# Optimization experiments

Hardware: AMD Instinct MI355X
Metric: run time of the kernel (lower is better)

## Reference

```python
import jax, jax.numpy as jnp
import numpy as np

EPS = 1e-10
COMMITMENT_COST = 0.25


def setup_inputs() -> dict:
    key = jax.random.key(0)
    k1, k2, k3, k4 = jax.random.split(key, 4)
    return {
        "x": jax.random.normal(k1, (32, 64, 64, 64), dtype=jnp.float32),  # NCHW, C=D=64
        "emb0": jax.random.normal(k2, (512, 64), dtype=jnp.float32),
        "emb1": jax.random.normal(k3, (512, 64), dtype=jnp.float32),
        "emb2": jax.random.normal(k4, (512, 64), dtype=jnp.float32),
        "idx": 1,
    }


def reference(x, emb0, emb1, emb2, idx):
    # NCHW -> NHWC, flatten to [N, D]
    inputs = jnp.transpose(x, (0, 2, 3, 1))
    in_shape = inputs.shape
    D = in_shape[-1]
    flat = inputs.reshape(-1, D)  # [N, D]

    if idx == 0:
        codes = emb0
    elif idx == 1:
        codes = jnp.concatenate([emb0, emb1], axis=0)
    else:
        codes = jnp.concatenate([emb0, emb2], axis=0)  # [K, D]

    distances = (
        jnp.sum(flat * flat, axis=1, keepdims=True)
        + jnp.sum(codes * codes, axis=1)
        - 2.0 * jnp.matmul(flat, codes.T)
    )
    enc_idx = jnp.argmin(distances, axis=1)  # [N]

    # one-hot @ codes is just a gather
    quantized = codes[enc_idx].reshape(in_shape)

    e_latent_loss = jnp.mean((jax.lax.stop_gradient(quantized) - inputs) ** 2)
    q_latent_loss = jnp.mean((quantized - jax.lax.stop_gradient(inputs)) ** 2)
    loss = q_latent_loss + COMMITMENT_COST * e_latent_loss

    # straight-through estimator
    quantized_st = inputs + jax.lax.stop_gradient(quantized - inputs)

    K = codes.shape[0]
    N = flat.shape[0]
    avg_probs = jnp.zeros((K,), dtype=flat.dtype).at[enc_idx].add(1.0) / N
    perplexity = jnp.exp(-jnp.sum(avg_probs * jnp.log(avg_probs + EPS)))

    return jnp.transpose(quantized_st, (0, 3, 1, 2)), loss, perplexity
```

## Files before the change

### kernel.cpp

```cpp
#include <hip/hip_runtime.h>
#include <math.h>

#define NROWS   131072
#define DFEAT   64
#define KHALF   512
#define HW      4096
#define CHW     262144
#define NQOUT   8388608
#define NBLK    512

typedef __attribute__((ext_vector_type(8))) short   bf16x8;
typedef __attribute__((ext_vector_type(4))) float   f32x4;

__device__ __forceinline__ unsigned short f2bf(float f) {
    unsigned int u = __float_as_uint(f);
    u += 0x7FFFu + ((u >> 16) & 1u);
    return (unsigned short)(u >> 16);
}
__device__ __forceinline__ float bf2f(unsigned short h) {
    return __uint_as_float(((unsigned int)h) << 16);
}

__global__ void vq_prep(const float* __restrict__ e0, const float* __restrict__ e1,
                        const float* __restrict__ e2, const int* __restrict__ idxp,
                        float* __restrict__ wsf, float* __restrict__ cnh,
                        unsigned short* __restrict__ fragbuf) {
    int tau = blockIdx.x * 256 + threadIdx.x;
    if (tau < 1536) wsf[tau] = 0.f;

    int idx = idxp[0];
    const float* sel = (idx == 2) ? e2 : e1;

    if (tau < 1024) {
        const float* row = (tau < KHALF) ? (e0 + (size_t)tau * DFEAT)
                                         : (sel + (size_t)(tau - KHALF) * DFEAT);
        float s = 0.f;
#pragma unroll
        for (int c = 0; c < DFEAT; ++c) s = fmaf(row[c], row[c], s);
        cnh[tau] = 0.5f * s;
    }

    int tile = tau >> 8;
    int rem  = tau & 255;
    int f    = rem >> 6;
    int L    = rem & 63;
    int code = tile * 16 + (L & 15);
    int kb   = (f & 1) * 32 + (L >> 4) * 8;
    int lo_f = f >> 1;
    const float* src = (code < KHALF) ? (e0 + (size_t)code * DFEAT)
                                      : (sel + (size_t)(code - KHALF) * DFEAT);
    unsigned short* dst = fragbuf + (size_t)tau * 8;
#pragma unroll
    for (int j = 0; j < 8; ++j) {
        float v = src[kb + j];
        unsigned short hb = f2bf(v);
        dst[j] = lo_f ? f2bf(v - bf2f(hb)) : hb;
    }
}

#define TILE_STEP(BC0, BC1, BC2, BC3, CNC, BN0, BN1, BN2, BN3, CNN, TT, TL)   \
    {                                                                          \
        const int tl_ = (TL);                                                  \
        BN0 = fb[(tl_ * 4 + 0) * 64 + L];                                      \
        BN1 = fb[(tl_ * 4 + 1) * 64 + L];                                      \
        BN2 = fb[(tl_ * 4 + 2) * 64 + L];                                      \
        BN3 = fb[(tl_ * 4 + 3) * 64 + L];                                      \
        CNN = cnh[tl_ * 16 + m];                                               \
        const int kt_ = (TT) * 16 + m;                                         \
        _Pragma("unroll")                                                      \
        for (int rt = 0; rt < 4; ++rt) {                                       \
            f32x4 acc = {0.f, 0.f, 0.f, 0.f};                                  \
            acc = __builtin_amdgcn_mfma_f32_16x16x32_bf16(ahi[rt][0], BC0, acc, 0, 0, 0); \
            acc = __builtin_amdgcn_mfma_f32_16x16x32_bf16(ahi[rt][1], BC1, acc, 0, 0, 0); \
            acc = __builtin_amdgcn_mfma_f32_16x16x32_bf16(ahi[rt][0], BC2, acc, 0, 0, 0); \
            acc = __builtin_amdgcn_mfma_f32_16x16x32_bf16(ahi[rt][1], BC3, acc, 0, 0, 0); \
            acc = __builtin_amdgcn_mfma_f32_16x16x32_bf16(alo[rt][0], BC0, acc, 0, 0, 0); \
            acc = __builtin_amdgcn_mfma_f32_16x16x32_bf16(alo[rt][1], BC1, acc, 0, 0, 0); \
            acc = __builtin_amdgcn_mfma_f32_16x16x32_bf16(alo[rt][0], BC2, acc, 0, 0, 0); \
            acc = __builtin_amdgcn_mfma_f32_16x16x32_bf16(alo[rt][1], BC3, acc, 0, 0, 0); \
            _Pragma("unroll")                                                  \
            for (int r = 0; r < 4; ++r) {                                      \
                float s = acc[r] - CNC;                                        \
                if (s > best[rt * 4 + r]) { best[rt * 4 + r] = s; bidx[rt * 4 + r] = kt_; } \
            }                                                                  \
        }                                                                      \
    }

__global__ __launch_bounds__(256, 2) void vq_main(
        const float* __restrict__ x,
        const float* __restrict__ e0, const float* __restrict__ e1,
        const float* __restrict__ e2, const int* __restrict__ idxp,
        const float* __restrict__ cnh, const unsigned short* __restrict__ fragbuf,
        float* __restrict__ out, float* __restrict__ loss_acc,
        int* __restrict__ hist) {
    __shared__ float xsq_s[256];
    __shared__ float sc_s[256];
    __shared__ int   bk_s[256];

    const int t = threadIdx.x;
    const int w = t >> 6;
    const int L = t & 63;
    const int q = L >> 4;
    const int m = L & 15;

    const int rowbase = blockIdx.x * 256;
    const int n  = rowbase >> 12;
    const int s0 = rowbase & 4095;

    const int idx = idxp[0];
    const float* sel = (idx == 2) ? e2 : e1;
    const int ntiles = (idx == 0) ? 32 : 64;

    bf16x8 ahi[4][2], alo[4][2];
    const float* xb = x + (size_t)n * CHW + (s0 + w * 64);
#pragma unroll
    for (int rt = 0; rt < 4; ++rt) {
        const float* xr = xb + rt * 16 + m;
        float xs = 0.f;
#pragma unroll
        for (int h = 0; h < 2; ++h) {
#pragma unroll
            for (int j = 0; j < 8; ++j) {
                int c = h * 32 + q * 8 + j;
                float v = xr[(size_t)c * HW];
                xs = fmaf(v, v, xs);
                unsigned short hb = f2bf(v);
                unsigned short lb = f2bf(v - bf2f(hb));
                ahi[rt][h][j] = (short)hb;
                alo[rt][h][j] = (short)lb;
            }
        }
        xs += __shfl_xor(xs, 16, 64);
        xs += __shfl_xor(xs, 32, 64);
        if (q == 0) xsq_s[w * 64 + rt * 16 + m] = xs;
    }

    const bf16x8* fb = (const bf16x8*)fragbuf;
    float best[16];
    int   bidx[16];
#pragma unroll
    for (int i = 0; i < 16; ++i) { best[i] = -3.4e38f; bidx[i] = 0; }

    bf16x8 X0 = fb[0 * 64 + L];
    bf16x8 X1 = fb[1 * 64 + L];
    bf16x8 X2 = fb[2 * 64 + L];
    bf16x8 X3 = fb[3 * 64 + L];
    float  Xc = cnh[m];
    bf16x8 Y0, Y1, Y2, Y3;
    float  Yc;

    for (int tt = 0; tt < ntiles; tt += 2) {
        TILE_STEP(X0, X1, X2, X3, Xc, Y0, Y1, Y2, Y3, Yc, tt, tt + 1);
        const int t2 = (tt + 2 < ntiles) ? tt + 2 : ntiles - 1;
        TILE_STEP(Y0, Y1, Y2, Y3, Yc, X0, X1, X2, X3, Xc, tt + 1, t2);
    }

#pragma unroll
    for (int i = 0; i < 16; ++i) {
        float b = best[i]; int k = bidx[i];
#pragma unroll
        for (int off = 1; off < 16; off <<= 1) {
            float ob = __shfl_xor(b, off, 64);
            int   ok = __shfl_xor(k, off, 64);
            if (ob > b || (ob == b && ok < k)) { b = ob; k = ok; }
        }
        if (m == 0) {
            int row = w * 64 + (i >> 2) * 16 + q * 4 + (i & 3);
            sc_s[row] = b; bk_s[row] = k;
        }
    }
    __syncthreads();

    const int k   = bk_s[t];
    float dist    = xsq_s[t] - 2.f * sc_s[t];
    float l = dist;
#pragma unroll
    for (int off = 32; off > 0; off >>= 1) l += __shfl_down(l, off, 64);
    if (L == 0) atomicAdd(loss_acc, l);
    atomicAdd(&hist[k], 1);

    const float* cp = (k < KHALF) ? (e0 + (size_t)k * DFEAT)
                                  : (sel + (size_t)(k - KHALF) * DFEAT);
    const float4* cp4 = (const float4*)cp;
    float* op = out + (size_t)n * CHW + (s0 + t);
#pragma unroll
    for (int c4 = 0; c4 < 16; ++c4) {
        float4 v = cp4[c4];
        op[(size_t)(4 * c4 + 0) * HW] = v.x;
        op[(size_t)(4 * c4 + 1) * HW] = v.y;
        op[(size_t)(4 * c4 + 2) * HW] = v.z;
        op[(size_t)(4 * c4 + 3) * HW] = v.w;
    }
}

__global__ void vq_finalize(const float* __restrict__ wsf, const int* __restrict__ hist,
                            float* __restrict__ out) {
    __shared__ double partial[16];
    const int t = threadIdx.x;
    double p = (double)hist[t] / (double)NROWS;
    double term = p * log(p + 1e-10);
#pragma unroll
    for (int off = 32; off > 0; off >>= 1) term += __shfl_down(term, off, 64);
    if ((t & 63) == 0) partial[t >> 6] = term;
    __syncthreads();
    if (t == 0) {
        double s = 0.0;
        for (int i = 0; i < 16; ++i) s += partial[i];
        out[NQOUT + 1] = (float)exp(-s);
        out[NQOUT]     = 1.25f * (wsf[0] / (float)NQOUT);
    }
}

extern "C" void kernel_launch(void* const* d_in, const int* in_sizes, int n_in,
                              void* d_out, int out_size, void* d_ws, size_t ws_size,
                              hipStream_t stream) {
    const float* x  = (const float*)d_in[0];
    const float* e0 = (const float*)d_in[1];
    const float* e1 = (const float*)d_in[2];
    const float* e2 = (const float*)d_in[3];
    const int* idxp = (const int*)d_in[4];
    float* out = (float*)d_out;

    float* wsf      = (float*)d_ws;
    float* loss_acc = wsf;
    int*   hist     = (int*)(wsf + 256);
    float* cnh      = wsf + 2048;
    unsigned short* fragbuf = (unsigned short*)(wsf + 4096);

    vq_prep<<<64, 256, 0, stream>>>(e0, e1, e2, idxp, wsf, cnh, fragbuf);
    vq_main<<<NBLK, 256, 0, stream>>>(x, e0, e1, e2, idxp, cnh, fragbuf,
                                      out, loss_acc, hist);
    vq_finalize<<<1, 1024, 0, stream>>>(wsf, hist, out);
}
```

Measured before the change: 183.5 us.

## Split codebook scan across two wave groups per block and merge argmin

```diff
diff --git a/kernel.cpp b/kernel.cpp
--- a/kernel.cpp
+++ b/kernel.cpp
@@ -86,7 +86,7 @@
         }                                                                      \
     }
 
-__global__ __launch_bounds__(256, 2) void vq_main(
+__global__ __launch_bounds__(512, 4) void vq_main(
         const float* __restrict__ x,
         const float* __restrict__ e0, const float* __restrict__ e1,
         const float* __restrict__ e2, const int* __restrict__ idxp,
@@ -94,14 +94,16 @@
         float* __restrict__ out, float* __restrict__ loss_acc,
         int* __restrict__ hist) {
     __shared__ float xsq_s[256];
-    __shared__ float sc_s[256];
-    __shared__ int   bk_s[256];
-
-    const int t = threadIdx.x;
-    const int w = t >> 6;
-    const int L = t & 63;
-    const int q = L >> 4;
-    const int m = L & 15;
+    __shared__ float sc_s[512];
+    __shared__ int   bk_s[512];
+
+    const int t  = threadIdx.x;
+    const int w  = t >> 6;
+    const int wg = w >> 2;
+    const int wv = w & 3;
+    const int L  = t & 63;
+    const int q  = L >> 4;
+    const int m  = L & 15;
 
     const int rowbase = blockIdx.x * 256;
     const int n  = rowbase >> 12;
@@ -110,9 +112,11 @@
     const int idx = idxp[0];
     const float* sel = (idx == 2) ? e2 : e1;
     const int ntiles = (idx == 0) ? 32 : 64;
+    const int nt2 = ntiles >> 1;
+    const int t0 = wg * nt2;
 
     bf16x8 ahi[4][2], alo[4][2];
-    const float* xb = x + (size_t)n * CHW + (s0 + w * 64);
+    const float* xb = x + (size_t)n * CHW + (s0 + wv * 64);
 #pragma unroll
     for (int rt = 0; rt < 4; ++rt) {
         const float* xr = xb + rt * 16 + m;
@@ -132,7 +136,7 @@
         }
         xs += __shfl_xor(xs, 16, 64);
         xs += __shfl_xor(xs, 32, 64);
-        if (q == 0) xsq_s[w * 64 + rt * 16 + m] = xs;
+        if (wg == 0 && q == 0) xsq_s[wv * 64 + rt * 16 + m] = xs;
     }
 
     const bf16x8* fb = (const bf16x8*)fragbuf;
@@ -141,17 +145,17 @@
 #pragma unroll
     for (int i = 0; i < 16; ++i) { best[i] = -3.4e38f; bidx[i] = 0; }
 
-    bf16x8 X0 = fb[0 * 64 + L];
-    bf16x8 X1 = fb[1 * 64 + L];
-    bf16x8 X2 = fb[2 * 64 + L];
-    bf16x8 X3 = fb[3 * 64 + L];
-    float  Xc = cnh[m];
+    bf16x8 X0 = fb[(t0 * 4 + 0) * 64 + L];
+    bf16x8 X1 = fb[(t0 * 4 + 1) * 64 + L];
+    bf16x8 X2 = fb[(t0 * 4 + 2) * 64 + L];
+    bf16x8 X3 = fb[(t0 * 4 + 3) * 64 + L];
+    float  Xc = cnh[t0 * 16 + m];
     bf16x8 Y0, Y1, Y2, Y3;
     float  Yc;
 
-    for (int tt = 0; tt < ntiles; tt += 2) {
+    for (int tt = t0; tt < t0 + nt2; tt += 2) {
         TILE_STEP(X0, X1, X2, X3, Xc, Y0, Y1, Y2, Y3, Yc, tt, tt + 1);
-        const int t2 = (tt + 2 < ntiles) ? tt + 2 : ntiles - 1;
+        const int t2 = (tt + 2 < t0 + nt2) ? tt + 2 : t0 + nt2 - 1;
         TILE_STEP(Y0, Y1, Y2, Y3, Yc, X0, X1, X2, X3, Xc, tt + 1, t2);
     }
 
@@ -165,31 +169,44 @@
             if (ob > b || (ob == b && ok < k)) { b = ob; k = ok; }
         }
         if (m == 0) {
-            int row = w * 64 + (i >> 2) * 16 + q * 4 + (i & 3);
-            sc_s[row] = b; bk_s[row] = k;
+            int row = wv * 64 + (i >> 2) * 16 + q * 4 + (i & 3);
+            sc_s[wg * 256 + row] = b; bk_s[wg * 256 + row] = k;
         }
     }
     __syncthreads();
 
-    const int k   = bk_s[t];
-    float dist    = xsq_s[t] - 2.f * sc_s[t];
-    float l = dist;
-#pragma unroll
-    for (int off = 32; off > 0; off >>= 1) l += __shfl_down(l, off, 64);
-    if (L == 0) atomicAdd(loss_acc, l);
-    atomicAdd(&hist[k], 1);
-
-    const float* cp = (k < KHALF) ? (e0 + (size_t)k * DFEAT)
-                                  : (sel + (size_t)(k - KHALF) * DFEAT);
-    const float4* cp4 = (const float4*)cp;
-    float* op = out + (size_t)n * CHW + (s0 + t);
-#pragma unroll
-    for (int c4 = 0; c4 < 16; ++c4) {
-        float4 v = cp4[c4];
-        op[(size_t)(4 * c4 + 0) * HW] = v.x;
-        op[(size_t)(4 * c4 + 1) * HW] = v.y;
-        op[(size_t)(4 * c4 + 2) * HW] = v.z;
-        op[(size_t)(4 * c4 + 3) * HW] = v.w;
+    if (t < 256) {
+        float sA = sc_s[t];       int kA = bk_s[t];
+        float sB = sc_s[256 + t]; int kB = bk_s[256 + t];
+        int   k  = (sB > sA) ? kB : kA;
+        float sc = (sB > sA) ? sB : sA;
+        bk_s[t] = k;
+        float dist = xsq_s[t] - 2.f * sc;
+        float l = dist;
+#pragma unroll
+        for (int off = 32; off > 0; off >>= 1) l += __shfl_down(l, off, 64);
+        if (L == 0) atomicAdd(loss_acc, l);
+        atomicAdd(&hist[k], 1);
+    }
+    __syncthreads();
+
+    {
+        const int row  = t & 255;
+        const int half = t >> 8;
+        const int k = bk_s[row];
+        const float* cp = ((k < KHALF) ? (e0 + (size_t)k * DFEAT)
+                                       : (sel + (size_t)(k - KHALF) * DFEAT)) + half * 32;
+        const float4* cp4 = (const float4*)cp;
+        float* op = out + (size_t)n * CHW + (s0 + row);
+#pragma unroll
+        for (int c4 = 0; c4 < 8; ++c4) {
+            float4 v = cp4[c4];
+            int c = half * 32 + 4 * c4;
+            op[(size_t)(c + 0) * HW] = v.x;
+            op[(size_t)(c + 1) * HW] = v.y;
+            op[(size_t)(c + 2) * HW] = v.z;
+            op[(size_t)(c + 3) * HW] = v.w;
+        }
     }
 }
 
@@ -228,7 +245,7 @@
     unsigned short* fragbuf = (unsigned short*)(wsf + 4096);
 
     vq_prep<<<64, 256, 0, stream>>>(e0, e1, e2, idxp, wsf, cnh, fragbuf);
-    vq_main<<<NBLK, 256, 0, stream>>>(x, e0, e1, e2, idxp, cnh, fragbuf,
+    vq_main<<<NBLK, 512, 0, stream>>>(x, e0, e1, e2, idxp, cnh, fragbuf,
                                       out, loss_acc, hist);
     vq_finalize<<<1, 1024, 0, stream>>>(wsf, hist, out);
 }
```

New measurement: 322.1 us. 75.5% more time.
